# Kernel optimization log

Measured on AMD Instinct MI355X. Metric: run time of the kernel, lower is better.

Reference implementation:

```python
import jax, jax.numpy as jnp
import numpy as np
from jax import lax

EPS = 1e-6
NUM_HEADS = 16
BSZ = 4


def _expected_alignment_train(p_choose):
    """p_choose: [B, T, S] -> alpha [B, T, S].
    q_ij = (1-p_{i,j-1}) q_{i,j-1} + a_{i-1,j};  a_ij = p_ij q_ij
    Per-step closed form: a_i = p_i * excl_cumprod(1-p_i) * cumsum(a_{i-1} / excl_cumprod_clamped)
    """
    B, T, S = p_choose.shape
    # safe exclusive cumprod of (1 - p) along src (fairseq exclusive_cumprod with eps clamp)
    one_minus_p = jnp.clip(1.0 - p_choose, EPS, 1.0)
    cp = jnp.cumprod(one_minus_p, axis=2)
    cumprod_1mp = jnp.concatenate([jnp.ones_like(cp[:, :, :1]), cp[:, :, :-1]], axis=2)
    cumprod_1mp_clamp = jnp.clip(cumprod_1mp, EPS, 1.0)

    init_attn = jnp.zeros((B, S), p_choose.dtype).at[:, 0].set(1.0)

    def step(prev_attn, xs):
        p_i, cp_i, cpc_i = xs  # each [B, S]
        alpha_i = jnp.clip(p_i * cp_i * jnp.cumsum(prev_attn / cpc_i, axis=1), 0.0, 1.0)
        return alpha_i, alpha_i

    xs = (jnp.swapaxes(p_choose, 0, 1),
          jnp.swapaxes(cumprod_1mp, 0, 1),
          jnp.swapaxes(cumprod_1mp_clamp, 0, 1))  # [T, B, S]
    _, alpha = lax.scan(step, init_attn, xs)
    alpha = jnp.swapaxes(alpha, 0, 1)  # [B, T, S]

    # mass preservation (no key padding): residual mass onto last source token
    residuals = 1.0 - jnp.clip(jnp.sum(alpha[:, :, :-1], axis=-1), 0.0, 1.0)
    alpha = alpha.at[:, :, -1].set(residuals)
    return alpha


def reference(q_proj, q_proj_dummy=None, *, _unused=None):
    raise NotImplementedError


def reference(q_proj, k_proj, v_proj, out_w, out_b, energy_bias):
    # q_proj/k_proj/v_proj: [bsz*num_heads, len, head_dim]
    energy = jnp.einsum('btd,bsd->bts', q_proj, k_proj) + energy_bias[0]
    p_choose = jax.nn.sigmoid(energy)                       # [B, T, S]
    alpha = _expected_alignment_train(p_choose)
    beta = alpha                                            # hard-aligned: expected_attention = alpha
    attn = jnp.einsum('bts,bsd->btd', beta, v_proj)         # [B, T, head_dim]
    BH, T, D = attn.shape
    attn = jnp.swapaxes(attn, 0, 1).reshape(T, BSZ, NUM_HEADS * D)  # [T, bsz, embed]
    out = attn @ out_w.T + out_b                            # out_proj
    return out, alpha


def setup_inputs():
    key = jax.random.key(0)
    ks = jax.random.split(key, 4)
    BH, T, S, D = 64, 1024, 1024, 64
    E = NUM_HEADS * D
    return {
        'q_proj': jax.random.normal(ks[0], (BH, T, D), jnp.float32) * 0.1,
        'k_proj': jax.random.normal(ks[1], (BH, S, D), jnp.float32) * 0.1,
        'v_proj': jax.random.normal(ks[2], (BH, S, D), jnp.float32),
        'out_w': jax.random.normal(ks[3], (E, E), jnp.float32) * 0.02,
        'out_b': jnp.zeros((E,), jnp.float32),
        'energy_bias': jnp.full((1,), -2.0, jnp.float32),
    }
```

## Files before the change

kernel.cpp:

```cpp
#include <hip/hip_runtime.h>

#define TT 1024
#define SSZ 1024
#define DD 64
#define BHN 64
#define BSZN 4
#define EEN 1024
#define EPSF 1e-6f

using f32x4 = __attribute__((ext_vector_type(4))) float;
using i32x2 = __attribute__((ext_vector_type(2))) int;
using i32x4 = __attribute__((ext_vector_type(4))) int;
using s16x8 = __attribute__((ext_vector_type(8))) short;

__device__ unsigned short g_Qb[(size_t)BHN * TT * SSZ];
__device__ unsigned short g_Pb[(size_t)BHN * TT * SSZ];
__device__ unsigned short g_Vt[(size_t)BHN * DD * SSZ];
__device__ unsigned short g_Wb[(size_t)EEN * EEN];
__device__ unsigned short g_Xb[(size_t)TT * BSZN * EEN];

template<int CTRL, int RM>
__device__ __forceinline__ float f_dpp(float x, float ident) {
  return __builtin_bit_cast(float,
      __builtin_amdgcn_update_dpp(__builtin_bit_cast(int, ident),
                                  __builtin_bit_cast(int, x),
                                  CTRL, RM, 0xF, false));
}

__device__ __forceinline__ float wscan_add(float x) {
  x += f_dpp<0x111, 0xF>(x, 0.0f);
  x += f_dpp<0x112, 0xF>(x, 0.0f);
  x += f_dpp<0x114, 0xF>(x, 0.0f);
  x += f_dpp<0x118, 0xF>(x, 0.0f);
  x += f_dpp<0x142, 0xA>(x, 0.0f);
  x += f_dpp<0x143, 0xC>(x, 0.0f);
  return x;
}

__device__ __forceinline__ float wave_shr1(float x, float ident) {
  return f_dpp<0x138, 0xF>(x, ident);
}

__device__ __forceinline__ i32x2 aload2(const unsigned short* p) {
  i32x2 r;
  asm volatile("global_load_dwordx2 %0, %1, off" : "=v"(r) : "v"(p));
  return r;
}
__device__ __forceinline__ void astore(float* p, f32x4 v) {
  asm volatile("global_store_dwordx4 %0, %1, off" :: "v"(p), "v"(v) : "memory");
}
__device__ __forceinline__ void astore2(unsigned short* p, i32x2 v) {
  asm volatile("global_store_dwordx2 %0, %1, off" :: "v"(p), "v"(v) : "memory");
}

__device__ __forceinline__ int cvt_pk(float lo, float hi) {
  int r;
  asm("v_cvt_pk_bf16_f32 %0, %1, %2" : "=v"(r) : "v"(lo), "v"(hi));
  return r;
}
__device__ __forceinline__ unsigned short bfr(float x) {
  unsigned u = __builtin_bit_cast(unsigned, x);
  u += 0x7fffu + ((u >> 16) & 1u);
  return (unsigned short)(u >> 16);
}
__device__ __forceinline__ float bfl(int u) {
  return __builtin_bit_cast(float, u << 16);
}
__device__ __forceinline__ float bfh(int u) {
  return __builtin_bit_cast(float, (int)((unsigned)u & 0xffff0000u));
}
__device__ __forceinline__ s16x8 pack8p(const float* p) {
  f32x4 a = *(const f32x4*)p;
  f32x4 b = *(const f32x4*)(p + 4);
  i32x4 r;
  r[0] = cvt_pk(a[0], a[1]); r[1] = cvt_pk(a[2], a[3]);
  r[2] = cvt_pk(b[0], b[1]); r[3] = cvt_pk(b[2], b[3]);
  return __builtin_bit_cast(s16x8, r);
}
__device__ __forceinline__ s16x8 pack8f(float v0, float v1, float v2, float v3,
                                        float v4, float v5, float v6, float v7) {
  i32x4 r;
  r[0] = cvt_pk(v0, v1); r[1] = cvt_pk(v2, v3);
  r[2] = cvt_pk(v4, v5); r[3] = cvt_pk(v6, v7);
  return __builtin_bit_cast(s16x8, r);
}

__global__ __launch_bounds__(256) void k_prep_w(const float* __restrict__ W) {
  const size_t idx = ((size_t)blockIdx.x * 256 + threadIdx.x) * 8;
  *(s16x8*)(g_Wb + idx) = pack8p(W + idx);
}

__global__ __launch_bounds__(256) void k_prep_v(const float* __restrict__ V) {
  __shared__ float tile[64][65];
  const int tid = threadIdx.x;
  const int bh = blockIdx.x >> 4;
  const int s0 = (blockIdx.x & 15) << 6;
  {
    const int r = tid >> 2, cq = (tid & 3) << 4;
    const float* src = V + ((size_t)bh * SSZ + s0 + r) * DD + cq;
    *(float4*)&tile[r][cq + 0]  = *(const float4*)(src + 0);
    *(float4*)&tile[r][cq + 4]  = *(const float4*)(src + 4);
    *(float4*)&tile[r][cq + 8]  = *(const float4*)(src + 8);
    *(float4*)&tile[r][cq + 12] = *(const float4*)(src + 12);
  }
  __syncthreads();
  {
    const int d = tid >> 2, sq = (tid & 3) << 4;
    const int s1 = s0 + sq, s2 = s1 + 8;
    unsigned short* d0 = g_Vt + ((size_t)(bh * 32 + (s1 >> 5)) * DD + d) * 32 + (s1 & 31);
    unsigned short* d1 = g_Vt + ((size_t)(bh * 32 + (s2 >> 5)) * DD + d) * 32 + (s2 & 31);
    *(s16x8*)d0 = pack8f(tile[sq + 0][d], tile[sq + 1][d], tile[sq + 2][d], tile[sq + 3][d],
                         tile[sq + 4][d], tile[sq + 5][d], tile[sq + 6][d], tile[sq + 7][d]);
    *(s16x8*)d1 = pack8f(tile[sq + 8][d], tile[sq + 9][d], tile[sq + 10][d], tile[sq + 11][d],
                         tile[sq + 12][d], tile[sq + 13][d], tile[sq + 14][d], tile[sq + 15][d]);
  }
}

__global__ __launch_bounds__(256) void k_energy(const float* __restrict__ Q,
                                                const float* __restrict__ Kp,
                                                const float* __restrict__ eb) {
  const int tid = threadIdx.x, w = tid >> 6, l = tid & 63;
  const int rl = l & 15, kg = l >> 4;
  const int bh = blockIdx.x >> 6;
  const int tile = blockIdx.x & 63;
  const int m0 = (tile >> 2) << 6;
  const int n0 = (((tile & 3) << 2) + w) << 6;
  const float* qb = Q + (size_t)bh * TT * DD;
  const float* kb = Kp + (size_t)bh * SSZ * DD;

  f32x4 acc[4][4];
#pragma unroll
  for (int i = 0; i < 4; ++i)
#pragma unroll
    for (int j = 0; j < 4; ++j) acc[i][j] = (f32x4)0.0f;

#pragma unroll
  for (int ks = 0; ks < 2; ++ks) {
    const int kof = (ks << 5) + (kg << 3);
    s16x8 af[4], bf[4];
#pragma unroll
    for (int fi = 0; fi < 4; ++fi)
      af[fi] = pack8p(qb + (size_t)(m0 + fi * 16 + rl) * DD + kof);
#pragma unroll
    for (int fj = 0; fj < 4; ++fj)
      bf[fj] = pack8p(kb + (size_t)(n0 + fj * 16 + rl) * DD + kof);
#pragma unroll
    for (int fi = 0; fi < 4; ++fi)
#pragma unroll
      for (int fj = 0; fj < 4; ++fj)
        acc[fi][fj] = __builtin_amdgcn_mfma_f32_16x16x32_bf16(af[fi], bf[fj], acc[fi][fj], 0, 0, 0);
  }

  const float bias = eb[0];
  unsigned short* pb = g_Qb + (size_t)bh * TT * SSZ;
#pragma unroll
  for (int fi = 0; fi < 4; ++fi)
#pragma unroll
    for (int r = 0; r < 4; ++r) {
      const size_t rowoff = (size_t)(m0 + fi * 16 + (kg << 2) + r) * SSZ;
#pragma unroll
      for (int fj = 0; fj < 4; ++fj) {
        float x = acc[fi][fj][r] + bias;
        float s = __builtin_amdgcn_rcpf(1.0f + __expf(-x));
        pb[rowoff + n0 + fj * 16 + rl] = bfr(s);
      }
    }
}

#define STEP(T, QS) do {                                                       \
  const int t_ = (T);                                                          \
  asm volatile("s_waitcnt vmcnt(8)" ::: "memory");                             \
  __builtin_amdgcn_sched_barrier(0);                                           \
  float fn0 = 1.0f - bfl(QS[0]);                                               \
  float fn1 = 1.0f - bfh(QS[0]);                                               \
  float fn2 = 1.0f - bfl(QS[1]);                                               \
  float fn3 = 1.0f - bfh(QS[1]);                                               \
  { int rr = t_ + 5; if (rr > TT - 1) rr = TT - 1;                             \
    QS = aload2(gqe + (size_t)rr * SSZ); }                                     \
  float ln0 = fn0, ln1 = ln0 * fn1, ln2 = ln1 * fn2, ln3 = ln2 * fn3;          \
  float An0 = ln3;                                                             \
  float An1 = An0 * f_dpp<0x111, 0xF>(An0, 1.0f);                              \
  float An2 = An1 * f_dpp<0x112, 0xF>(An1, 1.0f);                              \
  float An3 = An2 * f_dpp<0x114, 0xF>(An2, 1.0f);                              \
  float An4 = An3 * f_dpp<0x118, 0xF>(An3, 1.0f);                              \
  float An5 = An4 * f_dpp<0x142, 0xA>(An4, 1.0f);                              \
  float An6 = An5 * f_dpp<0x143, 0xC>(An5, 1.0f);                              \
  float wEn = wave_shr1(An6, 1.0f);                                            \
  float bb0 = fminf(c0  * prev0, prev0);                                       \
  float bb1 = fminf(cl0 * prev1, prev1);                                       \
  float bb2 = fminf(cl1 * prev2, prev2);                                       \
  float bb3 = fminf(cl2 * prev3, prev3);                                       \
  float Blo1 = fmaf(fc0, bb0, bb1);                                            \
  float Blo2 = fmaf(fc1, Blo1, bb2);                                           \
  float Blo3 = fmaf(fc2, Blo2, bb3);                                           \
  float B_ = fc3 * Blo3;                                                       \
  B_ = fmaf(As0, f_dpp<0x111, 0xF>(B_, 0.0f), B_);                             \
  B_ = fmaf(As1, f_dpp<0x112, 0xF>(B_, 0.0f), B_);                             \
  B_ = fmaf(As2, f_dpp<0x114, 0xF>(B_, 0.0f), B_);                             \
  B_ = fmaf(As3, f_dpp<0x118, 0xF>(B_, 0.0f), B_);                             \
  B_ = fmaf(As4, f_dpp<0x142, 0xA>(B_, 0.0f), B_);                             \
  float Bfull = fmaf(As5, f_dpp<0x143, 0xC>(B_, 0.0f), B_);                    \
  float wB = wave_shr1(Bfull, 0.0f);                                           \
  if (lane == 63) ldsAB[t_ & 1][w] = make_float2(An6, Bfull);                  \
  asm volatile("s_waitcnt lgkmcnt(0)" ::: "memory");                           \
  __builtin_amdgcn_s_barrier();                                                \
  __builtin_amdgcn_sched_barrier(0);                                           \
  float2 ab0 = ldsAB[t_ & 1][0];                                               \
  float2 ab1 = ldsAB[t_ & 1][1];                                               \
  float2 ab2 = ldsAB[t_ & 1][2];                                               \
  float Ew = 0.0f;                                                             \
  if (w == 1) Ew = ab0.y;                                                      \
  else if (w == 2) Ew = fmaf(A1g, ab0.y, ab1.y);                               \
  else if (w == 3) Ew = fmaf(A2g, fmaf(A1g, ab0.y, ab1.y), ab2.y);             \
  float El = fmaf(wE, Ew, wB);                                                 \
  float D0 = bb0 + El;                                                         \
  float D1 = fmaf(lc0, El, Blo1);                                              \
  float D2 = fmaf(lc1, El, Blo2);                                              \
  float D3 = fmaf(lc2, El, Blo3);                                              \
  float a0 = fminf(fmaf(-fc0, D0, D0), 1.0f);                                  \
  float a1 = fminf(fmaf(-fc1, D1, D1), 1.0f);                                  \
  float a2 = fminf(fmaf(-fc2, D2, D2), 1.0f);                                  \
  float a3 = fminf(fmaf(-fc3, D3, D3), 1.0f);                                  \
  prev0 = a0; prev1 = a1; prev2 = a2; prev3 = a3;                              \
  f32x4 av4; av4.x = a0; av4.y = a1; av4.z = a2; av4.w = a3;                   \
  if (tid != 255) {                                                            \
    astore(gq + (size_t)t_ * SSZ, av4);                                        \
    i32x2 pk; pk[0] = cvt_pk(a0, a1); pk[1] = cvt_pk(a2, a3);                  \
    astore2(gpb + (size_t)t_ * 32, pk);                                        \
  }                                                                            \
  float la = (a0 + a1) + (a2 + a3);                                            \
  float wsum = wscan_add(la);                                                  \
  if (lane == 63 && w < 3) ldsS[t_ & 1][w] = wsum;                             \
  if (tid == 255) {                                                            \
    if (t_ > 0) {                                                              \
      float tot = ldsS[(t_ - 1) & 1][0] + ldsS[(t_ - 1) & 1][1]                \
                + ldsS[(t_ - 1) & 1][2] + wsum_prev;                           \
      float rest = tot - pend.w;                                               \
      pend.w = 1.0f - fminf(fmaxf(rest, 0.0f), 1.0f);                          \
      astore(gq + (size_t)(t_ - 1) * SSZ, pend);                               \
      i32x2 pk2; pk2[0] = cvt_pk(pend.x, pend.y); pk2[1] = cvt_pk(pend.z, pend.w); \
      astore2(gpb + (size_t)(t_ - 1) * 32, pk2);                               \
    }                                                                          \
    pend = av4; wsum_prev = wsum;                                              \
  }                                                                            \
  fc0 = fn0; fc1 = fn1; fc2 = fn2; fc3 = fn3;                                  \
  lc0 = ln0; lc1 = ln1; lc2 = ln2;                                             \
  As0 = An0; As1 = An1; As2 = An2; As3 = An3; As4 = An4; As5 = An5;            \
  wE = wEn;                                                                    \
  float Pw_ = 1.0f;                                                            \
  if (w > 0) Pw_ = ab0.x;                                                      \
  if (w > 1) Pw_ *= ab1.x;                                                     \
  if (w > 2) Pw_ *= ab2.x;                                                     \
  c0 = (Pw_ * 1e6f) * wEn;                                                     \
  cl0 = c0 * ln0; cl1 = c0 * ln1; cl2 = c0 * ln2;                              \
  A1g = ab1.x; A2g = ab2.x;                                                    \
} while (0)

__global__ __launch_bounds__(256, 1) void k_scan(float* __restrict__ A) {
  const int b = blockIdx.x;
  const int tid = threadIdx.x;
  const int w = tid >> 6;
  const int lane = tid & 63;
  __shared__ float2 ldsAB[2][4];
  __shared__ float ldsS[2][4];

  float* gq = A + (size_t)b * TT * SSZ + ((size_t)w << 8) + ((size_t)lane << 2);
  const unsigned short* gqe = g_Qb + (size_t)b * TT * SSZ + ((size_t)w << 8) + ((size_t)lane << 2);
  const int sb = (w << 3) + (lane >> 3);
  unsigned short* gpb = g_Pb + ((size_t)(b * 32 + sb) * TT) * 32 + ((lane & 7) << 2);

  i32x2 q0 = aload2(gqe + (size_t)0 * SSZ);
  i32x2 q1 = aload2(gqe + (size_t)1 * SSZ);
  i32x2 q2 = aload2(gqe + (size_t)2 * SSZ);
  i32x2 q3 = aload2(gqe + (size_t)3 * SSZ);
  asm volatile("s_waitcnt vmcnt(0)" ::: "memory");
  __builtin_amdgcn_sched_barrier(0);

  float fc0 = 1.0f - bfl(q0[0]);
  float fc1 = 1.0f - bfh(q0[0]);
  float fc2 = 1.0f - bfl(q0[1]);
  float fc3 = 1.0f - bfh(q0[1]);
  q0 = aload2(gqe + (size_t)4 * SSZ);
  float lc0 = fc0, lc1 = lc0 * fc1, lc2 = lc1 * fc2;
  float lc3 = lc2 * fc3;
  float As0 = lc3;
  float As1 = As0 * f_dpp<0x111, 0xF>(As0, 1.0f);
  float As2 = As1 * f_dpp<0x112, 0xF>(As1, 1.0f);
  float As3 = As2 * f_dpp<0x114, 0xF>(As2, 1.0f);
  float As4 = As3 * f_dpp<0x118, 0xF>(As3, 1.0f);
  float As5 = As4 * f_dpp<0x142, 0xA>(As4, 1.0f);
  float A6  = As5 * f_dpp<0x143, 0xC>(As5, 1.0f);
  float wE = wave_shr1(A6, 1.0f);
  if (lane == 63) ldsAB[1][w] = make_float2(A6, 0.0f);
  asm volatile("s_waitcnt lgkmcnt(0)" ::: "memory");
  __builtin_amdgcn_s_barrier();
  __builtin_amdgcn_sched_barrier(0);
  float2 pab0 = ldsAB[1][0], pab1 = ldsAB[1][1], pab2 = ldsAB[1][2];
  float A1g = pab1.x, A2g = pab2.x;
  float Pw = 1.0f;
  if (w > 0) Pw = pab0.x;
  if (w > 1) Pw *= pab1.x;
  if (w > 2) Pw *= pab2.x;
  float c0 = (Pw * 1e6f) * wE;
  float cl0 = c0 * lc0, cl1 = c0 * lc1, cl2 = c0 * lc2;

  float prev0 = (tid == 0) ? 1.0f : 0.0f;
  float prev1 = 0.0f, prev2 = 0.0f, prev3 = 0.0f;
  f32x4 pend; pend.x = 0.0f; pend.y = 0.0f; pend.z = 0.0f; pend.w = 0.0f;
  float wsum_prev = 0.0f;

  for (int t0 = 0; t0 < TT; t0 += 4) {
    STEP(t0 + 0, q1);
    STEP(t0 + 1, q2);
    STEP(t0 + 2, q3);
    STEP(t0 + 3, q0);
  }

  asm volatile("s_waitcnt lgkmcnt(0)" ::: "memory");
  __builtin_amdgcn_s_barrier();
  __builtin_amdgcn_sched_barrier(0);
  if (tid == 255) {
    float tot = ldsS[(TT - 1) & 1][0] + ldsS[(TT - 1) & 1][1]
              + ldsS[(TT - 1) & 1][2] + wsum_prev;
    float rest = tot - pend.w;
    pend.w = 1.0f - fminf(fmaxf(rest, 0.0f), 1.0f);
    astore(gq + (size_t)(TT - 1) * SSZ, pend);
    i32x2 pk; pk[0] = cvt_pk(pend.x, pend.y); pk[1] = cvt_pk(pend.z, pend.w);
    astore2(gpb + (size_t)(TT - 1) * 32, pk);
  }
}

__global__ __launch_bounds__(256) void k_av() {
  const int tid = threadIdx.x, w = tid >> 6, l = tid & 63;
  const int rl = l & 15, kg = l >> 4;
  const int gw = blockIdx.x * 4 + w;
  const int bh = gw >> 6;
  const int t0 = (gw & 63) << 4;

  const unsigned short* ab = g_Pb + ((size_t)(bh * 32) * TT + (t0 + rl)) * 32 + (kg << 3);
  const unsigned short* vb = g_Vt + ((size_t)(bh * 32) * DD + rl) * 32 + (kg << 3);

  f32x4 acc[4];
#pragma unroll
  for (int j = 0; j < 4; ++j) acc[j] = (f32x4)0.0f;

  for (int kk = 0; kk < 32; ++kk) {
    s16x8 a = *(const s16x8*)(ab + (size_t)kk * TT * 32);
#pragma unroll
    for (int fj = 0; fj < 4; ++fj) {
      s16x8 b = *(const s16x8*)(vb + ((size_t)kk * DD + fj * 16) * 32);
      acc[fj] = __builtin_amdgcn_mfma_f32_16x16x32_bf16(a, b, acc[fj], 0, 0, 0);
    }
  }

  const int bz = bh >> 4, hh = bh & 15;
#pragma unroll
  for (int fj = 0; fj < 4; ++fj) {
    const int e = hh * DD + fj * 16 + rl;
    const size_t ebase = ((size_t)(e >> 5) * (TT * BSZN)) * 32 + (e & 31);
#pragma unroll
    for (int r = 0; r < 4; ++r) {
      const int m = (t0 + (kg << 2) + r) * BSZN + bz;
      g_Xb[ebase + (size_t)m * 32] = bfr(acc[fj][r]);
    }
  }
}

__global__ __launch_bounds__(256) void k_out(const float* __restrict__ Bb,
                                             float* __restrict__ Out) {
  const int tid = threadIdx.x, w = tid >> 6, l = tid & 63;
  const int rl = l & 15, kg = l >> 4;
  const int gw = blockIdx.x * 4 + w;
  const int m0 = (gw >> 4) << 4;
  const int n0 = (gw & 15) << 6;

  const unsigned short* xb = g_Xb + (size_t)(m0 + rl) * 32 + (kg << 3);

  f32x4 acc[4];
#pragma unroll
  for (int j = 0; j < 4; ++j) acc[j] = (f32x4)0.0f;

  for (int kk = 0; kk < 32; ++kk) {
    s16x8 a = *(const s16x8*)(xb + (size_t)kk * (TT * BSZN) * 32);
    const int kof = (kk << 5) + (kg << 3);
#pragma unroll
    for (int fj = 0; fj < 4; ++fj) {
      s16x8 b = *(const s16x8*)(g_Wb + (size_t)(n0 + fj * 16 + rl) * EEN + kof);
      acc[fj] = __builtin_amdgcn_mfma_f32_16x16x32_bf16(a, b, acc[fj], 0, 0, 0);
    }
  }

#pragma unroll
  for (int fj = 0; fj < 4; ++fj) {
    const float bias = Bb[n0 + fj * 16 + rl];
#pragma unroll
    for (int r = 0; r < 4; ++r) {
      const int m = m0 + (kg << 2) + r;
      Out[(size_t)m * EEN + n0 + fj * 16 + rl] = acc[fj][r] + bias;
    }
  }
}

extern "C" void kernel_launch(void* const* d_in, const int* in_sizes, int n_in,
                              void* d_out, int out_size, void* d_ws, size_t ws_size,
                              hipStream_t stream) {
  const float* Q  = (const float*)d_in[0];
  const float* K  = (const float*)d_in[1];
  const float* V  = (const float*)d_in[2];
  const float* W  = (const float*)d_in[3];
  const float* Bb = (const float*)d_in[4];
  const float* eb = (const float*)d_in[5];
  float* Out = (float*)d_out;
  float* Alpha = Out + (size_t)TT * BSZN * EEN;

  k_prep_w<<<dim3(512), dim3(256), 0, stream>>>(W);
  k_prep_v<<<dim3(BHN * 16), dim3(256), 0, stream>>>(V);
  k_energy<<<dim3(BHN * 64), dim3(256), 0, stream>>>(Q, K, eb);
  k_scan<<<dim3(BHN), dim3(256), 0, stream>>>(Alpha);
  k_av<<<dim3(1024), dim3(256), 0, stream>>>();
  k_out<<<dim3(1024), dim3(256), 0, stream>>>(Bb, Out);
}
```

Measured before the change: 700.1 us.

## Widen scan block to 512 threads with two source elements per lane

The sequential alignment scan now uses 8 waves per block, each lane owning 2 source positions instead of 4. This halves the per-lane serial work in each time step and extends the cross-wave carry combination to 7 preceding waves. The trade-off is a longer cross-wave LDS read and carry chain per step, plus a barrier across twice as many waves. Per-lane loads and stores become narrower (single dword instead of dwordx2/dwordx4).

```diff
diff --git a/kernel.cpp b/kernel.cpp
--- a/kernel.cpp
+++ b/kernel.cpp
@@ -8,6 +8,7 @@
 #define EEN 1024
 #define EPSF 1e-6f
 
+using f32x2 = __attribute__((ext_vector_type(2))) float;
 using f32x4 = __attribute__((ext_vector_type(4))) float;
 using i32x2 = __attribute__((ext_vector_type(2))) int;
 using i32x4 = __attribute__((ext_vector_type(4))) int;
@@ -41,16 +42,16 @@
   return f_dpp<0x138, 0xF>(x, ident);
 }
 
-__device__ __forceinline__ i32x2 aload2(const unsigned short* p) {
-  i32x2 r;
-  asm volatile("global_load_dwordx2 %0, %1, off" : "=v"(r) : "v"(p));
+__device__ __forceinline__ int aload1(const unsigned short* p) {
+  int r;
+  asm volatile("global_load_dword %0, %1, off" : "=v"(r) : "v"(p));
   return r;
 }
-__device__ __forceinline__ void astore(float* p, f32x4 v) {
-  asm volatile("global_store_dwordx4 %0, %1, off" :: "v"(p), "v"(v) : "memory");
-}
-__device__ __forceinline__ void astore2(unsigned short* p, i32x2 v) {
+__device__ __forceinline__ void astore2f(float* p, f32x2 v) {
   asm volatile("global_store_dwordx2 %0, %1, off" :: "v"(p), "v"(v) : "memory");
+}
+__device__ __forceinline__ void astore1(unsigned short* p, int v) {
+  asm volatile("global_store_dword %0, %1, off" :: "v"(p), "v"(v) : "memory");
 }
 
 __device__ __forceinline__ int cvt_pk(float lo, float hi) {
@@ -171,14 +172,12 @@
   const int t_ = (T);                                                          \
   asm volatile("s_waitcnt vmcnt(8)" ::: "memory");                             \
   __builtin_amdgcn_sched_barrier(0);                                           \
-  float fn0 = 1.0f - bfl(QS[0]);                                               \
-  float fn1 = 1.0f - bfh(QS[0]);                                               \
-  float fn2 = 1.0f - bfl(QS[1]);                                               \
-  float fn3 = 1.0f - bfh(QS[1]);                                               \
+  float fn0 = 1.0f - bfl(QS);                                                  \
+  float fn1 = 1.0f - bfh(QS);                                                  \
   { int rr = t_ + 5; if (rr > TT - 1) rr = TT - 1;                             \
-    QS = aload2(gqe + (size_t)rr * SSZ); }                                     \
-  float ln0 = fn0, ln1 = ln0 * fn1, ln2 = ln1 * fn2, ln3 = ln2 * fn3;          \
-  float An0 = ln3;                                                             \
+    QS = aload1(gqe + (size_t)rr * SSZ); }                                     \
+  float ln0 = fn0, ln1 = ln0 * fn1;                                            \
+  float An0 = ln1;                                                             \
   float An1 = An0 * f_dpp<0x111, 0xF>(An0, 1.0f);                              \
   float An2 = An1 * f_dpp<0x112, 0xF>(An1, 1.0f);                              \
   float An3 = An2 * f_dpp<0x114, 0xF>(An2, 1.0f);                              \
@@ -188,12 +187,8 @@
   float wEn = wave_shr1(An6, 1.0f);                                            \
   float bb0 = fminf(c0  * prev0, prev0);                                       \
   float bb1 = fminf(cl0 * prev1, prev1);                                       \
-  float bb2 = fminf(cl1 * prev2, prev2);                                       \
-  float bb3 = fminf(cl2 * prev3, prev3);                                       \
   float Blo1 = fmaf(fc0, bb0, bb1);                                            \
-  float Blo2 = fmaf(fc1, Blo1, bb2);                                           \
-  float Blo3 = fmaf(fc2, Blo2, bb3);                                           \
-  float B_ = fc3 * Blo3;                                                       \
+  float B_ = fc1 * Blo1;                                                       \
   B_ = fmaf(As0, f_dpp<0x111, 0xF>(B_, 0.0f), B_);                             \
   B_ = fmaf(As1, f_dpp<0x112, 0xF>(B_, 0.0f), B_);                             \
   B_ = fmaf(As2, f_dpp<0x114, 0xF>(B_, 0.0f), B_);                             \
@@ -208,82 +203,91 @@
   float2 ab0 = ldsAB[t_ & 1][0];                                               \
   float2 ab1 = ldsAB[t_ & 1][1];                                               \
   float2 ab2 = ldsAB[t_ & 1][2];                                               \
+  float2 ab3 = ldsAB[t_ & 1][3];                                               \
+  float2 ab4 = ldsAB[t_ & 1][4];                                               \
+  float2 ab5 = ldsAB[t_ & 1][5];                                               \
+  float2 ab6 = ldsAB[t_ & 1][6];                                               \
+  float e = ab0.y;                                                             \
   float Ew = 0.0f;                                                             \
-  if (w == 1) Ew = ab0.y;                                                      \
-  else if (w == 2) Ew = fmaf(A1g, ab0.y, ab1.y);                               \
-  else if (w == 3) Ew = fmaf(A2g, fmaf(A1g, ab0.y, ab1.y), ab2.y);             \
+  if (w == 1) Ew = e;                                                          \
+  e = fmaf(Ag1, e, ab1.y); if (w == 2) Ew = e;                                 \
+  e = fmaf(Ag2, e, ab2.y); if (w == 3) Ew = e;                                 \
+  e = fmaf(Ag3, e, ab3.y); if (w == 4) Ew = e;                                 \
+  e = fmaf(Ag4, e, ab4.y); if (w == 5) Ew = e;                                 \
+  e = fmaf(Ag5, e, ab5.y); if (w == 6) Ew = e;                                 \
+  e = fmaf(Ag6, e, ab6.y); if (w == 7) Ew = e;                                 \
   float El = fmaf(wE, Ew, wB);                                                 \
   float D0 = bb0 + El;                                                         \
   float D1 = fmaf(lc0, El, Blo1);                                              \
-  float D2 = fmaf(lc1, El, Blo2);                                              \
-  float D3 = fmaf(lc2, El, Blo3);                                              \
   float a0 = fminf(fmaf(-fc0, D0, D0), 1.0f);                                  \
   float a1 = fminf(fmaf(-fc1, D1, D1), 1.0f);                                  \
-  float a2 = fminf(fmaf(-fc2, D2, D2), 1.0f);                                  \
-  float a3 = fminf(fmaf(-fc3, D3, D3), 1.0f);                                  \
-  prev0 = a0; prev1 = a1; prev2 = a2; prev3 = a3;                              \
-  f32x4 av4; av4.x = a0; av4.y = a1; av4.z = a2; av4.w = a3;                   \
-  if (tid != 255) {                                                            \
-    astore(gq + (size_t)t_ * SSZ, av4);                                        \
-    i32x2 pk; pk[0] = cvt_pk(a0, a1); pk[1] = cvt_pk(a2, a3);                  \
-    astore2(gpb + (size_t)t_ * 32, pk);                                        \
+  prev0 = a0; prev1 = a1;                                                      \
+  if (tid != 511) {                                                            \
+    f32x2 av; av[0] = a0; av[1] = a1;                                          \
+    astore2f(gq + (size_t)t_ * SSZ, av);                                       \
+    astore1(gpb + (size_t)t_ * 32, cvt_pk(a0, a1));                            \
   }                                                                            \
-  float la = (a0 + a1) + (a2 + a3);                                            \
-  float wsum = wscan_add(la);                                                  \
-  if (lane == 63 && w < 3) ldsS[t_ & 1][w] = wsum;                             \
-  if (tid == 255) {                                                            \
+  float wsum = wscan_add(a0 + a1);                                             \
+  if (lane == 63 && w < 7) ldsS[t_ & 1][w] = wsum;                             \
+  if (tid == 511) {                                                            \
     if (t_ > 0) {                                                              \
-      float tot = ldsS[(t_ - 1) & 1][0] + ldsS[(t_ - 1) & 1][1]                \
-                + ldsS[(t_ - 1) & 1][2] + wsum_prev;                           \
-      float rest = tot - pend.w;                                               \
-      pend.w = 1.0f - fminf(fmaxf(rest, 0.0f), 1.0f);                          \
-      astore(gq + (size_t)(t_ - 1) * SSZ, pend);                               \
-      i32x2 pk2; pk2[0] = cvt_pk(pend.x, pend.y); pk2[1] = cvt_pk(pend.z, pend.w); \
-      astore2(gpb + (size_t)(t_ - 1) * 32, pk2);                               \
+      const int p_ = (t_ - 1) & 1;                                             \
+      float tot = ((ldsS[p_][0] + ldsS[p_][1]) + (ldsS[p_][2] + ldsS[p_][3]))  \
+                + ((ldsS[p_][4] + ldsS[p_][5]) + ldsS[p_][6]) + wsum_prev;     \
+      float rest = tot - pend1;                                                \
+      pend1 = 1.0f - fminf(fmaxf(rest, 0.0f), 1.0f);                           \
+      f32x2 pv; pv[0] = pend0; pv[1] = pend1;                                  \
+      astore2f(gq + (size_t)(t_ - 1) * SSZ, pv);                               \
+      astore1(gpb + (size_t)(t_ - 1) * 32, cvt_pk(pend0, pend1));              \
     }                                                                          \
-    pend = av4; wsum_prev = wsum;                                              \
+    pend0 = a0; pend1 = a1; wsum_prev = wsum;                                  \
   }                                                                            \
-  fc0 = fn0; fc1 = fn1; fc2 = fn2; fc3 = fn3;                                  \
-  lc0 = ln0; lc1 = ln1; lc2 = ln2;                                             \
+  fc0 = fn0; fc1 = fn1; lc0 = ln0;                                             \
   As0 = An0; As1 = An1; As2 = An2; As3 = An3; As4 = An4; As5 = An5;            \
   wE = wEn;                                                                    \
+  Ag1 = ab1.x; Ag2 = ab2.x; Ag3 = ab3.x;                                       \
+  Ag4 = ab4.x; Ag5 = ab5.x; Ag6 = ab6.x;                                       \
+  float p1 = ab0.x;                                                            \
+  float p2 = p1 * ab1.x;                                                       \
+  float p3 = p2 * ab2.x;                                                       \
+  float p4 = p3 * ab3.x;                                                       \
+  float p5 = p4 * ab4.x;                                                       \
+  float p6 = p5 * ab5.x;                                                       \
+  float p7 = p6 * ab6.x;                                                       \
   float Pw_ = 1.0f;                                                            \
-  if (w > 0) Pw_ = ab0.x;                                                      \
-  if (w > 1) Pw_ *= ab1.x;                                                     \
-  if (w > 2) Pw_ *= ab2.x;                                                     \
+  if (w == 1) Pw_ = p1; else if (w == 2) Pw_ = p2; else if (w == 3) Pw_ = p3;  \
+  else if (w == 4) Pw_ = p4; else if (w == 5) Pw_ = p5;                        \
+  else if (w == 6) Pw_ = p6; else if (w == 7) Pw_ = p7;                        \
   c0 = (Pw_ * 1e6f) * wEn;                                                     \
-  cl0 = c0 * ln0; cl1 = c0 * ln1; cl2 = c0 * ln2;                              \
-  A1g = ab1.x; A2g = ab2.x;                                                    \
+  cl0 = c0 * ln0;                                                              \
 } while (0)
 
-__global__ __launch_bounds__(256, 1) void k_scan(float* __restrict__ A) {
+__global__ __launch_bounds__(512, 1) void k_scan(float* __restrict__ A) {
   const int b = blockIdx.x;
   const int tid = threadIdx.x;
   const int w = tid >> 6;
   const int lane = tid & 63;
-  __shared__ float2 ldsAB[2][4];
-  __shared__ float ldsS[2][4];
-
-  float* gq = A + (size_t)b * TT * SSZ + ((size_t)w << 8) + ((size_t)lane << 2);
-  const unsigned short* gqe = g_Qb + (size_t)b * TT * SSZ + ((size_t)w << 8) + ((size_t)lane << 2);
-  const int sb = (w << 3) + (lane >> 3);
-  unsigned short* gpb = g_Pb + ((size_t)(b * 32 + sb) * TT) * 32 + ((lane & 7) << 2);
-
-  i32x2 q0 = aload2(gqe + (size_t)0 * SSZ);
-  i32x2 q1 = aload2(gqe + (size_t)1 * SSZ);
-  i32x2 q2 = aload2(gqe + (size_t)2 * SSZ);
-  i32x2 q3 = aload2(gqe + (size_t)3 * SSZ);
+  __shared__ float2 ldsAB[2][8];
+  __shared__ float ldsS[2][8];
+
+  float* gq = A + (size_t)b * TT * SSZ + ((size_t)w << 7) + ((size_t)lane << 1);
+  const unsigned short* gqe = g_Qb + (size_t)b * TT * SSZ + ((size_t)w << 7) + ((size_t)lane << 1);
+  const int sb = (w << 2) + (lane >> 4);
+  unsigned short* gpb = g_Pb + ((size_t)(b * 32 + sb) * TT) * 32 + ((lane & 15) << 1);
+
+  int q0 = aload1(gqe + (size_t)0 * SSZ);
+  int q1 = aload1(gqe + (size_t)1 * SSZ);
+  int q2 = aload1(gqe + (size_t)2 * SSZ);
+  int q3 = aload1(gqe + (size_t)3 * SSZ);
   asm volatile("s_waitcnt vmcnt(0)" ::: "memory");
   __builtin_amdgcn_sched_barrier(0);
 
-  float fc0 = 1.0f - bfl(q0[0]);
-  float fc1 = 1.0f - bfh(q0[0]);
-  float fc2 = 1.0f - bfl(q0[1]);
-  float fc3 = 1.0f - bfh(q0[1]);
-  q0 = aload2(gqe + (size_t)4 * SSZ);
-  float lc0 = fc0, lc1 = lc0 * fc1, lc2 = lc1 * fc2;
-  float lc3 = lc2 * fc3;
-  float As0 = lc3;
+  float fc0 = 1.0f - bfl(q0);
+  float fc1 = 1.0f - bfh(q0);
+  q0 = aload1(gqe + (size_t)4 * SSZ);
+  float lc0 = fc0;
+  float lc1 = lc0 * fc1;
+  float As0 = lc1;
   float As1 = As0 * f_dpp<0x111, 0xF>(As0, 1.0f);
   float As2 = As1 * f_dpp<0x112, 0xF>(As1, 1.0f);
   float As3 = As2 * f_dpp<0x114, 0xF>(As2, 1.0f);
@@ -295,18 +299,30 @@
   asm volatile("s_waitcnt lgkmcnt(0)" ::: "memory");
   __builtin_amdgcn_s_barrier();
   __builtin_amdgcn_sched_barrier(0);
-  float2 pab0 = ldsAB[1][0], pab1 = ldsAB[1][1], pab2 = ldsAB[1][2];
-  float A1g = pab1.x, A2g = pab2.x;
+  float2 pb0 = ldsAB[1][0], pb1 = ldsAB[1][1], pb2 = ldsAB[1][2];
+  float2 pb3 = ldsAB[1][3], pb4 = ldsAB[1][4], pb5 = ldsAB[1][5];
+  float2 pb6 = ldsAB[1][6];
+  float Ag1 = pb1.x, Ag2 = pb2.x, Ag3 = pb3.x;
+  float Ag4 = pb4.x, Ag5 = pb5.x, Ag6 = pb6.x;
+  {
+  }
+  float p1 = pb0.x;
+  float p2 = p1 * pb1.x;
+  float p3 = p2 * pb2.x;
+  float p4 = p3 * pb3.x;
+  float p5 = p4 * pb4.x;
+  float p6 = p5 * pb5.x;
+  float p7 = p6 * pb6.x;
   float Pw = 1.0f;
-  if (w > 0) Pw = pab0.x;
-  if (w > 1) Pw *= pab1.x;
-  if (w > 2) Pw *= pab2.x;
+  if (w == 1) Pw = p1; else if (w == 2) Pw = p2; else if (w == 3) Pw = p3;
+  else if (w == 4) Pw = p4; else if (w == 5) Pw = p5;
+  else if (w == 6) Pw = p6; else if (w == 7) Pw = p7;
   float c0 = (Pw * 1e6f) * wE;
-  float cl0 = c0 * lc0, cl1 = c0 * lc1, cl2 = c0 * lc2;
+  float cl0 = c0 * lc0;
 
   float prev0 = (tid == 0) ? 1.0f : 0.0f;
-  float prev1 = 0.0f, prev2 = 0.0f, prev3 = 0.0f;
-  f32x4 pend; pend.x = 0.0f; pend.y = 0.0f; pend.z = 0.0f; pend.w = 0.0f;
+  float prev1 = 0.0f;
+  float pend0 = 0.0f, pend1 = 0.0f;
   float wsum_prev = 0.0f;
 
   for (int t0 = 0; t0 < TT; t0 += 4) {
@@ -319,14 +335,15 @@
   asm volatile("s_waitcnt lgkmcnt(0)" ::: "memory");
   __builtin_amdgcn_s_barrier();
   __builtin_amdgcn_sched_barrier(0);
-  if (tid == 255) {
-    float tot = ldsS[(TT - 1) & 1][0] + ldsS[(TT - 1) & 1][1]
-              + ldsS[(TT - 1) & 1][2] + wsum_prev;
-    float rest = tot - pend.w;
-    pend.w = 1.0f - fminf(fmaxf(rest, 0.0f), 1.0f);
-    astore(gq + (size_t)(TT - 1) * SSZ, pend);
-    i32x2 pk; pk[0] = cvt_pk(pend.x, pend.y); pk[1] = cvt_pk(pend.z, pend.w);
-    astore2(gpb + (size_t)(TT - 1) * 32, pk);
+  if (tid == 511) {
+    const int p_ = (TT - 1) & 1;
+    float tot = ((ldsS[p_][0] + ldsS[p_][1]) + (ldsS[p_][2] + ldsS[p_][3]))
+              + ((ldsS[p_][4] + ldsS[p_][5]) + ldsS[p_][6]) + wsum_prev;
+    float rest = tot - pend1;
+    pend1 = 1.0f - fminf(fmaxf(rest, 0.0f), 1.0f);
+    f32x2 pv; pv[0] = pend0; pv[1] = pend1;
+    astore2f(gq + (size_t)(TT - 1) * SSZ, pv);
+    astore1(gpb + (size_t)(TT - 1) * 32, cvt_pk(pend0, pend1));
   }
 }
 
@@ -416,7 +433,7 @@
   k_prep_w<<<dim3(512), dim3(256), 0, stream>>>(W);
   k_prep_v<<<dim3(BHN * 16), dim3(256), 0, stream>>>(V);
   k_energy<<<dim3(BHN * 64), dim3(256), 0, stream>>>(Q, K, eb);
-  k_scan<<<dim3(BHN), dim3(256), 0, stream>>>(Alpha);
+  k_scan<<<dim3(BHN), dim3(512), 0, stream>>>(Alpha);
   k_av<<<dim3(1024), dim3(256), 0, stream>>>();
   k_out<<<dim3(1024), dim3(256), 0, stream>>>(Bb, Out);
 }
```

After: 775.7 us. +10.8%, slower.
